# Kernel optimization log

Hardware: AMD Instinct MI355X
Metric: run time of the kernel (lower is better)

The kernel has to match this reference:

```python
import jax, jax.numpy as jnp
import numpy as np

EPS = 1e-07


def unfold(a, p):
    # torch F.unfold(a, p, padding=(p-1)//2, stride=1): [B,C,H,W] -> [B, C*p*p, H*W]
    B, C, H, W = a.shape
    pad = (p - 1) // 2
    ap = jnp.pad(a, ((0, 0), (0, 0), (pad, pad), (pad, pad)))
    # channel ordering is C-major then (kh, kw), matching torch unfold
    patches = jnp.stack([ap[:, :, i:i + H, j:j + W] for i in range(p) for j in range(p)], axis=2)
    return patches.reshape(B, C * p * p, H * W)


def linear_attn(q, k, x):
    # q:[B,h,l1,d1]  k:[B,h,l2,d1]  x:[B,h,l2,d2]
    l1, d1 = q.shape[-2:]
    l2, d2 = x.shape[-2:]
    kt = jnp.swapaxes(k, -2, -1)  # [B,h,d1,l2]
    if l1 * d1 * l2 + l1 * l2 * d2 <= d2 * l2 * d1 + d2 * d1 * l1:
        s = q @ kt                                        # [B,h,l1,l2]
        s = s / (s.sum(axis=-1, keepdims=True) + EPS)
        return s @ x
    else:
        out = q @ (kt @ x)                                # [B,h,l1,d2]
        denom = q @ kt.sum(axis=-1, keepdims=True) + EPS  # [B,h,l1,1]
        return out / denom


def setup_inputs() -> dict:
    key = jax.random.key(0)
    k1, k2, k3, k4, k5 = jax.random.split(key, 5)
    B, C, H, W = 4, 64, 128, 128
    x = jax.random.normal(k1, (B, C, H, W), dtype=jnp.float32)
    qkv_w = jax.random.normal(k2, (3 * C, C), dtype=jnp.float32) * 0.05
    qkv_b = jax.random.normal(k3, (3 * C,), dtype=jnp.float32) * 0.01
    proj_w = jax.random.normal(k4, (C, C, 3, 3), dtype=jnp.float32) * 0.05
    proj_b = jax.random.normal(k5, (C,), dtype=jnp.float32) * 0.01
    return {"x": x, "qkv_w": qkv_w, "qkv_b": qkv_b, "proj_w": proj_w, "proj_b": proj_b}


def reference(x, qkv_w, qkv_b, proj_w, proj_b):
    numHeads, patchSize = 8, 3
    B, C, H, W = x.shape
    L = H * W
    # 1x1 conv qkv
    qkv = jnp.einsum('bchw,oc->bohw', x, qkv_w) + qkv_b[None, :, None, None]
    q, k, v = qkv[:, :C], qkv[:, C:2 * C], qkv[:, 2 * C:]
    q = jax.nn.relu(q)
    k = jax.nn.relu(k)
    q = unfold(q, patchSize)  # [B, C*p*p, L]
    k = unfold(k, patchSize)
    v = v.reshape(B, C, L)
    d1 = C * patchSize * patchSize
    assert d1 % numHeads == 0  # chosen so replicate-pad branch is skipped
    q = jnp.swapaxes(q.reshape(B, numHeads, d1 // numHeads, L), -1, -2)   # [B,h,L,d1h]
    k = jnp.swapaxes(k.reshape(B, numHeads, d1 // numHeads, L), -1, -2)
    v = jnp.swapaxes(v.reshape(B, numHeads, C // numHeads, L), -1, -2)    # [B,h,L,d2h]
    out = linear_attn(q, k, v)                                            # [B,h,L,d2h]
    out = jnp.swapaxes(out, -1, -2).reshape(B, C, H, W)
    # 3x3 conv proj, padding 1
    out = jax.lax.conv_general_dilated(out, proj_w, window_strides=(1, 1), padding='SAME',
                                       dimension_numbers=('NCHW', 'OIHW', 'NCHW'))
    out = out + proj_b[None, :, None, None]
    return out
```

## Files before the change

### kernel.cpp

```cpp
#include <hip/hip_runtime.h>
#include <hip/hip_fp16.h>

#define LL 16384
#define HH 128
#define WW 128
#define CC 64
#define NH 8
#define EPSF 1e-7f
#define KVCHUNKS 32

typedef __attribute__((ext_vector_type(8))) _Float16 f16x8;
typedef __attribute__((ext_vector_type(4))) float f32x4;
typedef __attribute__((ext_vector_type(8))) unsigned short u16x8;

static __device__ __forceinline__ unsigned short f2h_bits(float v) {
    const _Float16 h = (_Float16)v;
    unsigned short b;
    __builtin_memcpy(&b, &h, 2);
    return b;
}
static __device__ __forceinline__ float h2f_u16(unsigned short s) {
    _Float16 h;
    __builtin_memcpy(&h, &s, 2);
    return (float)h;
}
static __device__ __forceinline__ float h2f_lo(unsigned int u) {
    return h2f_u16((unsigned short)(u & 0xffffu));
}
static __device__ __forceinline__ float h2f_hi(unsigned int u) {
    return h2f_u16((unsigned short)(u >> 16));
}

__global__ void qkv_kernel(const float* __restrict__ x, const float* __restrict__ w,
                           const float* __restrict__ bias,
                           unsigned short* __restrict__ q, unsigned short* __restrict__ k,
                           unsigned short* __restrict__ v) {
    const int pix0 = blockIdx.x * 128;
    const int b    = blockIdx.y;
    const int tid  = threadIdx.x;
    const int lane = tid & 63;
    const int wv   = tid >> 6;

    __shared__ _Float16 xh[128][72], xl[128][72];
    __shared__ unsigned short wspace[2 * 64 * 72];
    _Float16* whp = (_Float16*)wspace;
    _Float16* wlp = whp + 64 * 72;
    unsigned short* rep = wspace;

    {
        const float* xb = x + (size_t)b * CC * LL + pix0;
        for (int idx = tid; idx < 64 * 128; idx += 256) {
            const int ci = idx >> 7;
            const int px = idx & 127;
            const float vv = xb[(size_t)ci * LL + px];
            const _Float16 h = (_Float16)vv;
            xh[px][ci] = h;
            xl[px][ci] = (_Float16)(vv - (float)h);
        }
    }

    const int g8 = (lane >> 4) * 8;
    const int rl = lane & 15;

    for (int sec = 0; sec < 3; ++sec) {
        __syncthreads();
        {
            const float* wsec = w + (size_t)sec * 64 * 64;
            for (int idx = tid; idx < 64 * 64; idx += 256) {
                const int co = idx >> 6;
                const int ci = idx & 63;
                const float vv = wsec[co * 64 + ci];
                const _Float16 h = (_Float16)vv;
                whp[co * 72 + ci] = h;
                wlp[co * 72 + ci] = (_Float16)(vv - (float)h);
            }
        }
        __syncthreads();

        f32x4 acc[4][2];
#pragma unroll
        for (int ct = 0; ct < 4; ++ct)
#pragma unroll
            for (int pt = 0; pt < 2; ++pt) acc[ct][pt] = (f32x4)0.f;

#pragma unroll
        for (int ks = 0; ks < 2; ++ks) {
            const int kb = ks * 32 + g8;
            f16x8 ah[4], al[4], bh[2], bl[2];
#pragma unroll
            for (int ct = 0; ct < 4; ++ct) {
                ah[ct] = *(const f16x8*)&whp[(ct * 16 + rl) * 72 + kb];
                al[ct] = *(const f16x8*)&wlp[(ct * 16 + rl) * 72 + kb];
            }
#pragma unroll
            for (int pt = 0; pt < 2; ++pt) {
                bh[pt] = *(const f16x8*)&xh[wv * 32 + pt * 16 + rl][kb];
                bl[pt] = *(const f16x8*)&xl[wv * 32 + pt * 16 + rl][kb];
            }
#pragma unroll
            for (int ct = 0; ct < 4; ++ct)
#pragma unroll
                for (int pt = 0; pt < 2; ++pt) {
                    acc[ct][pt] = __builtin_amdgcn_mfma_f32_16x16x32_f16(ah[ct], bh[pt], acc[ct][pt], 0, 0, 0);
                    acc[ct][pt] = __builtin_amdgcn_mfma_f32_16x16x32_f16(ah[ct], bl[pt], acc[ct][pt], 0, 0, 0);
                    acc[ct][pt] = __builtin_amdgcn_mfma_f32_16x16x32_f16(al[ct], bh[pt], acc[ct][pt], 0, 0, 0);
                }
        }
        __syncthreads();

        const bool do_relu = (sec < 2);
#pragma unroll
        for (int ct = 0; ct < 4; ++ct) {
            const int co_b = ct * 16 + (lane >> 4) * 4;
#pragma unroll
            for (int pt = 0; pt < 2; ++pt) {
                const int pxl = wv * 32 + pt * 16 + rl;
#pragma unroll
                for (int j = 0; j < 4; ++j) {
                    const int co = co_b + j;
                    float val = acc[ct][pt][j] + bias[sec * 64 + co];
                    if (do_relu) val = fmaxf(val, 0.f);
                    rep[co * 128 + pxl] = f2h_bits(val);
                }
            }
        }
        __syncthreads();

        unsigned short* dst = ((sec == 0) ? q : (sec == 1) ? k : v) + (size_t)b * 64 * LL;
#pragma unroll
        for (int i = 0; i < 4; ++i) {
            const int slot = i * 256 + tid;
            const int co = slot >> 4;
            const int u4 = slot & 15;
            *(uint4*)(dst + (size_t)co * LL + pix0 + u4 * 8) = *(const uint4*)&rep[co * 128 + u4 * 8];
        }
    }
}

__global__ void kv_kernel(const unsigned short* __restrict__ k,
                          const unsigned short* __restrict__ v,
                          float* __restrict__ KVp) {
    const int chunk = blockIdx.x;
    const int h = blockIdx.y;
    const int b = blockIdx.z;
    const int tid = threadIdx.x;
    const int c  = tid >> 5;
    const int s  = tid & 31;
    const int half = s >> 4;
    const int sl   = s & 15;
    const int cpb  = half * 4;

    __shared__ float klds[8][6][130];

    {
        const unsigned short* kb = k + ((size_t)(b * 64) + 8 * h) * LL;
        for (int t = tid; t < 8 * 6 * 130; t += 256) {
            const int ch = t / 780;
            const int r1 = t - ch * 780;
            const int lr = r1 / 130;
            const int cx = r1 - lr * 130;
            const int gy = chunk * 4 + lr - 1;
            const int gx = cx - 1;
            const bool ok = (gy >= 0 && gy < HH && gx >= 0 && gx < WW);
            klds[ch][lr][cx] = ok ? h2f_u16(kb[(size_t)ch * LL + gy * WW + gx]) : 0.f;
        }
    }
    __syncthreads();

    const unsigned short* vbase = v + ((size_t)(b * 64) + 8 * h + cpb) * LL;

    float kv4[9][4] = {{0.f}};
    float ks[9] = {0.f};

    for (int r = 0; r < 4; ++r) {
        const int y = chunk * 4 + r;
        for (int g = 0; g < 4; ++g) {
            const int col0 = g * 32 + sl * 2;
            float va[4], vb2[4];
#pragma unroll
            for (int cp = 0; cp < 4; ++cp) {
                const unsigned int u = *(const unsigned int*)(vbase + (size_t)cp * LL + y * WW + col0);
                va[cp]  = h2f_lo(u);
                vb2[cp] = h2f_hi(u);
            }
            float kw[3][4];
#pragma unroll
            for (int dy = 0; dy < 3; ++dy)
#pragma unroll
                for (int dxx = 0; dxx < 4; ++dxx)
                    kw[dy][dxx] = klds[c][r + dy][col0 + dxx];
#pragma unroll
            for (int dy = 0; dy < 3; ++dy)
#pragma unroll
                for (int dx = 0; dx < 3; ++dx) {
                    const int p = dy * 3 + dx;
                    const float ka  = kw[dy][dx];
                    const float kb2 = kw[dy][dx + 1];
                    ks[p] += ka + kb2;
#pragma unroll
                    for (int cp = 0; cp < 4; ++cp)
                        kv4[p][cp] = fmaf(kb2, vb2[cp], fmaf(ka, va[cp], kv4[p][cp]));
                }
        }
    }

#pragma unroll
    for (int p = 0; p < 9; ++p) {
#pragma unroll
        for (int m = 8; m >= 1; m >>= 1) ks[p] += __shfl_xor(ks[p], m);
#pragma unroll
        for (int cp = 0; cp < 4; ++cp) {
#pragma unroll
            for (int m = 8; m >= 1; m >>= 1) kv4[p][cp] += __shfl_xor(kv4[p][cp], m);
        }
    }

    if (sl == 0) {
        float* dst = KVp + (((size_t)(b * NH + h) * KVCHUNKS) + chunk) * 648;
#pragma unroll
        for (int p = 0; p < 9; ++p) {
#pragma unroll
            for (int cp = 0; cp < 4; ++cp)
                dst[(c * 9 + p) * 8 + cpb + cp] = kv4[p][cp];
            if (half == 0) dst[576 + c * 9 + p] = ks[p];
        }
    }
}

__global__ void prep_kernel(const float* __restrict__ KVp,
                            float* __restrict__ KV, float* __restrict__ KS,
                            const float* __restrict__ w, unsigned short* __restrict__ wfrag) {
    if (blockIdx.x < 32) {
        const int bh = blockIdx.x;
        const float* src = KVp + (size_t)bh * KVCHUNKS * 648;
        for (int idx = threadIdx.x; idx < 648; idx += 256) {
            float s0 = 0.f, s1 = 0.f, s2 = 0.f, s3 = 0.f;
#pragma unroll
            for (int ch = 0; ch < KVCHUNKS; ch += 4) {
                s0 += src[(ch + 0) * 648 + idx];
                s1 += src[(ch + 1) * 648 + idx];
                s2 += src[(ch + 2) * 648 + idx];
                s3 += src[(ch + 3) * 648 + idx];
            }
            const float sum = (s0 + s1) + (s2 + s3);
            if (idx < 576) KV[(size_t)bh * 576 + idx] = sum;
            else           KS[(size_t)bh * 72 + (idx - 576)] = sum;
        }
    } else {
        const int idx = (blockIdx.x - 32) * 256 + threadIdx.x;
        const int kk = idx & 63;
        const int co = (idx >> 6) & 63;
        const int ks = idx >> 12;
        const int kg = ks * 64 + kk;
        const int ci = kg >> 4, tap = kg & 15;
        const float vv = (tap < 9) ? w[(co * 64 + ci) * 9 + tap] : 0.f;
        const int kx = (((kk >> 3) ^ (co & 7)) << 3) | (kk & 7);
        wfrag[((size_t)ks * 64 + co) * 64 + kx] = f2h_bits(vv);
    }
}

__global__ void attn_kernel(const unsigned short* __restrict__ q, const float* __restrict__ KV,
                            const float* __restrict__ KS, unsigned int* __restrict__ aofu) {
    const int y = blockIdx.x;
    const int h = blockIdx.y;
    const int b = blockIdx.z;
    const int t = threadIdx.x;

    float out0[8] = {0.f}, out1[8] = {0.f};
    float den0 = 0.f, den1 = 0.f;
    const int kvbase = (b * NH + h) * 8;
    const bool tlo = (t > 0), thi = (t < 63);

    for (int c = 0; c < 8; ++c) {
        const unsigned short* qc = q + ((size_t)(b * 64) + 8 * h + c) * LL;
        float qw[3][6];
#pragma unroll
        for (int dy = 0; dy < 3; ++dy) {
            const int yy = y + dy - 1;
            const bool yok = (yy >= 0 && yy < HH);
            const unsigned short* row = qc + yy * WW;
            const unsigned int u0 = (yok && tlo) ? *(const unsigned int*)(row + 2 * t - 2) : 0u;
            const unsigned int u1 = yok ? *(const unsigned int*)(row + 2 * t) : 0u;
            const unsigned int u2 = (yok && thi) ? *(const unsigned int*)(row + 2 * t + 2) : 0u;
            qw[dy][0] = h2f_lo(u0);  qw[dy][1] = h2f_hi(u0);
            qw[dy][2] = h2f_lo(u1);  qw[dy][3] = h2f_hi(u1);
            qw[dy][4] = h2f_lo(u2);  qw[dy][5] = h2f_hi(u2);
        }
        const float* kvr = KV + ((size_t)(kvbase + c) * 9) * 8;
        const float* ksr = KS + (size_t)(kvbase + c) * 9;
#pragma unroll
        for (int dy = 0; dy < 3; ++dy)
#pragma unroll
            for (int dx = 0; dx < 3; ++dx) {
                const int p = dy * 3 + dx;
                const float q0 = qw[dy][1 + dx];
                const float q1 = qw[dy][2 + dx];
                const float ksv = ksr[p];
                den0 = fmaf(q0, ksv, den0);
                den1 = fmaf(q1, ksv, den1);
#pragma unroll
                for (int cp = 0; cp < 8; ++cp) {
                    const float kvv = kvr[p * 8 + cp];
                    out0[cp] = fmaf(q0, kvv, out0[cp]);
                    out1[cp] = fmaf(q1, kvv, out1[cp]);
                }
            }
    }
    const float inv0 = 1.f / (den0 + EPSF);
    const float inv1 = 1.f / (den1 + EPSF);
    const int pixu = y * (WW / 2) + t;
#pragma unroll
    for (int cp = 0; cp < 8; ++cp) {
        const unsigned int lo = f2h_bits(out0[cp] * inv0);
        const unsigned int hi = f2h_bits(out1[cp] * inv1);
        aofu[((size_t)(b * 64) + h * 8 + cp) * (LL / 2) + pixu] = lo | (hi << 16);
    }
}

#define CONV_PREFETCH(KS)                                                        \
    do {                                                                         \
        if (tid < 128) {                                                         \
            const unsigned short* src_ = aofb + (size_t)((KS) * 4 + scis) * LL;  \
            pa0 = (oky0 && u0ok) ? *(const unsigned int*)(src_ + o_m - 2) : 0u;  \
            pa1 = oky0 ? *(const unsigned int*)(src_ + o_m) : 0u;                \
            pa2 = (oky0 && u2ok) ? *(const unsigned int*)(src_ + o_m + 2) : 0u;  \
            pb0 = u0ok ? *(const unsigned int*)(src_ + o_c - 2) : 0u;            \
            pb1 = *(const unsigned int*)(src_ + o_c);                            \
            pb2 = u2ok ? *(const unsigned int*)(src_ + o_c + 2) : 0u;            \
            pc0 = (oky2 && u0ok) ? *(const unsigned int*)(src_ + o_p - 2) : 0u;  \
            pc1 = oky2 ? *(const unsigned int*)(src_ + o_p) : 0u;                \
            pc2 = (oky2 && u2ok) ? *(const unsigned int*)(src_ + o_p + 2) : 0u;  \
        } else {                                                                 \
            const uint4* wsrc_ = (const uint4*)(wfrag + (size_t)(KS) * 4096);    \
            wf0 = wsrc_[wt];        wf1 = wsrc_[128 + wt];                       \
            wf2 = wsrc_[256 + wt];  wf3 = wsrc_[384 + wt];                       \
        }                                                                        \
    } while (0)

__global__ __launch_bounds__(256) void conv_kernel(const unsigned short* __restrict__ aof,
                                                   const unsigned short* __restrict__ wfrag,
                                                   const float* __restrict__ bias,
                                                   float* __restrict__ out) {
    const int bid = blockIdx.x;
    const int swz = (bid & 7) * 128 + (bid >> 3);
    const int b = swz >> 8;
    const int rem = swz & 255;
    const int y = rem >> 1;
    const int colbase = (rem & 1) * 64;
    const int tid = threadIdx.x;
    const int lane = tid & 63;
    const int wv = tid >> 6;
    const int rl = lane & 15;
    const int g  = lane >> 4;

    __shared__ unsigned short plds[2][64 * 64];
    __shared__ unsigned short wlds[2][64 * 64];

    f32x4 acc[4];
#pragma unroll
    for (int ct = 0; ct < 4; ++ct) acc[ct] = (f32x4)0.f;

    const int pair = tid & 31;
    const int scis = (tid >> 5) & 3;
    const int wt   = tid & 127;
    const int pxA  = pair * 2;
    const int pxB  = pxA + 1;

    const unsigned short* aofb = aof + (size_t)b * 64 * LL;
    const int xc0 = colbase + pxA;
    const int o_c = y * WW + xc0;
    const int o_m = o_c - WW;
    const int o_p = o_c + WW;
    const bool oky0 = (y > 0);
    const bool oky2 = (y < HH - 1);
    const bool u0ok = (xc0 >= 2);
    const bool u2ok = (xc0 + 3 < WW);
    const int xsA0 = (((2 * scis)     ^ (pxA & 7)) << 3);
    const int xsA1 = (((2 * scis + 1) ^ (pxA & 7)) << 3);
    const int xsB0 = (((2 * scis)     ^ (pxB & 7)) << 3);
    const int xsB1 = (((2 * scis + 1) ^ (pxB & 7)) << 3);

    unsigned int pa0, pa1, pa2, pb0, pb1, pb2, pc0, pc1, pc2;
    uint4 wf0, wf1, wf2, wf3;

    CONV_PREFETCH(0);

    for (int ks = 0; ks < 16; ++ks) {
        const int cur = ks & 1;
        if (tid < 128) {
            unsigned short ha[16], hb[16];
            ha[0] = (unsigned short)(pa0 >> 16);      ha[1] = (unsigned short)(pa1 & 0xffffu);  ha[2] = (unsigned short)(pa1 >> 16);
            ha[3] = (unsigned short)(pb0 >> 16);      ha[4] = (unsigned short)(pb1 & 0xffffu);  ha[5] = (unsigned short)(pb1 >> 16);
            ha[6] = (unsigned short)(pc0 >> 16);      ha[7] = (unsigned short)(pc1 & 0xffffu);  ha[8] = (unsigned short)(pc1 >> 16);
            hb[0] = (unsigned short)(pa1 & 0xffffu);  hb[1] = (unsigned short)(pa1 >> 16);      hb[2] = (unsigned short)(pa2 & 0xffffu);
            hb[3] = (unsigned short)(pb1 & 0xffffu);  hb[4] = (unsigned short)(pb1 >> 16);      hb[5] = (unsigned short)(pb2 & 0xffffu);
            hb[6] = (unsigned short)(pc1 & 0xffffu);  hb[7] = (unsigned short)(pc1 >> 16);      hb[8] = (unsigned short)(pc2 & 0xffffu);
#pragma unroll
            for (int j = 9; j < 16; ++j) { ha[j] = 0; hb[j] = 0; }
            *(u16x8*)&plds[cur][pxA * 64 + xsA0] = *(u16x8*)&ha[0];
            *(u16x8*)&plds[cur][pxA * 64 + xsA1] = *(u16x8*)&ha[8];
            *(u16x8*)&plds[cur][pxB * 64 + xsB0] = *(u16x8*)&hb[0];
            *(u16x8*)&plds[cur][pxB * 64 + xsB1] = *(u16x8*)&hb[8];
        } else {
            uint4* wdst = (uint4*)&wlds[cur][0];
            wdst[wt]        = wf0;
            wdst[128 + wt]  = wf1;
            wdst[256 + wt]  = wf2;
            wdst[384 + wt]  = wf3;
        }
        __syncthreads();
        if (ks < 15) CONV_PREFETCH(ks + 1);

#pragma unroll
        for (int ksub = 0; ksub < 2; ++ksub) {
            const int xs = (((ksub * 4 + g) ^ (rl & 7)) << 3);
            const int row = wv * 16 + rl;
            const f16x8 bh = *(const f16x8*)&plds[cur][row * 64 + xs];
#pragma unroll
            for (int ct = 0; ct < 4; ++ct) {
                const int rowa = ct * 16 + rl;
                const f16x8 ah = *(const f16x8*)&wlds[cur][rowa * 64 + xs];
                acc[ct] = __builtin_amdgcn_mfma_f32_16x16x32_f16(ah, bh, acc[ct], 0, 0, 0);
            }
        }
    }

#pragma unroll
    for (int ct = 0; ct < 4; ++ct) {
        const int co_b = ct * 16 + g * 4;
        const int px = colbase + wv * 16 + rl;
#pragma unroll
        for (int j = 0; j < 4; ++j) {
            const int co = co_b + j;
            out[((size_t)b * 64 + co) * LL + y * WW + px] = acc[ct][j] + bias[co];
        }
    }
}

extern "C" void kernel_launch(void* const* d_in, const int* in_sizes, int n_in,
                              void* d_out, int out_size, void* d_ws, size_t ws_size,
                              hipStream_t stream) {
    const float* x      = (const float*)d_in[0];
    const float* qkv_w  = (const float*)d_in[1];
    const float* qkv_b  = (const float*)d_in[2];
    const float* proj_w = (const float*)d_in[3];
    const float* proj_b = (const float*)d_in[4];
    float* out = (float*)d_out;
    float* ws  = (float*)d_ws;

    const size_t n1 = (size_t)4 * 64 * LL;
    unsigned short* qb  = (unsigned short*)ws;
    unsigned short* kb  = (unsigned short*)(ws + n1);
    unsigned short* vb  = (unsigned short*)(ws + 2 * n1);
    unsigned short* aof = (unsigned short*)(ws + 3 * n1);
    float* KV   = ws + 4 * n1;
    float* KS   = KV + 4 * 8 * 8 * 9 * 8;
    float* KVp  = KS + 4 * 8 * 8 * 9;
    unsigned short* wfrag = (unsigned short*)(KVp + (size_t)32 * KVCHUNKS * 648);

    qkv_kernel<<<dim3(128, 4), 256, 0, stream>>>(x, qkv_w, qkv_b, qb, kb, vb);
    kv_kernel<<<dim3(KVCHUNKS, NH, 4), 256, 0, stream>>>(kb, vb, KVp);
    prep_kernel<<<288, 256, 0, stream>>>(KVp, KV, KS, proj_w, wfrag);
    attn_kernel<<<dim3(128, NH, 4), 64, 0, stream>>>(qb, KV, KS, (unsigned int*)aof);
    conv_kernel<<<1024, 256, 0, stream>>>(aof, wfrag, proj_b, out);
}
```

Baseline: 96.96 us.

## Precompute split-fp16 QKV weights, vectorize x loads, reduce KV partials via atomics

```diff
diff --git a/kernel.cpp b/kernel.cpp
--- a/kernel.cpp
+++ b/kernel.cpp
@@ -31,7 +31,38 @@
     return h2f_u16((unsigned short)(u >> 16));
 }
 
-__global__ void qkv_kernel(const float* __restrict__ x, const float* __restrict__ w,
+__global__ void prep0_kernel(float* __restrict__ KVz,
+                             const float* __restrict__ pw, unsigned short* __restrict__ wfrag,
+                             const float* __restrict__ qw, unsigned short* __restrict__ wqkvf) {
+    const int bid = blockIdx.x;
+    if (bid < 81) {
+        KVz[bid * 256 + threadIdx.x] = 0.f;
+    } else if (bid < 337) {
+        const int idx = (bid - 81) * 256 + threadIdx.x;
+        const int kk = idx & 63;
+        const int co = (idx >> 6) & 63;
+        const int ks = idx >> 12;
+        const int kg = ks * 64 + kk;
+        const int ci = kg >> 4, tap = kg & 15;
+        const float vv = (tap < 9) ? pw[(co * 64 + ci) * 9 + tap] : 0.f;
+        const int kx = (((kk >> 3) ^ (co & 7)) << 3) | (kk & 7);
+        wfrag[((size_t)ks * 64 + co) * 64 + kx] = f2h_bits(vv);
+    } else {
+        const int idx = (bid - 337) * 256 + threadIdx.x;
+        const int hl = idx / 12288;
+        const int r  = idx - hl * 12288;
+        const int sec = r >> 12;
+        const int r2  = r & 4095;
+        const int co  = r2 >> 6;
+        const int ci  = r2 & 63;
+        const float vv = qw[(sec * 64 + co) * 64 + ci];
+        const _Float16 h = (_Float16)vv;
+        const float out = hl ? (vv - (float)h) : vv;
+        wqkvf[idx] = f2h_bits(out);
+    }
+}
+
+__global__ void qkv_kernel(const float* __restrict__ x, const unsigned short* __restrict__ wqkvf,
                            const float* __restrict__ bias,
                            unsigned short* __restrict__ q, unsigned short* __restrict__ k,
                            unsigned short* __restrict__ v) {
@@ -42,40 +73,36 @@
     const int wv   = tid >> 6;
 
     __shared__ _Float16 xh[128][72], xl[128][72];
-    __shared__ unsigned short wspace[2 * 64 * 72];
-    _Float16* whp = (_Float16*)wspace;
-    _Float16* wlp = whp + 64 * 72;
-    unsigned short* rep = wspace;
+    __shared__ unsigned short rep[64 * 128];
 
     {
         const float* xb = x + (size_t)b * CC * LL + pix0;
-        for (int idx = tid; idx < 64 * 128; idx += 256) {
-            const int ci = idx >> 7;
-            const int px = idx & 127;
-            const float vv = xb[(size_t)ci * LL + px];
-            const _Float16 h = (_Float16)vv;
-            xh[px][ci] = h;
-            xl[px][ci] = (_Float16)(vv - (float)h);
-        }
-    }
+        for (int i4 = tid; i4 < 2048; i4 += 256) {
+            const int ci = i4 >> 5;
+            const int px = (i4 & 31) * 4;
+            const float4 vv = *(const float4*)&xb[(size_t)ci * LL + px];
+            _Float16 h;
+            h = (_Float16)vv.x; xh[px + 0][ci] = h; xl[px + 0][ci] = (_Float16)(vv.x - (float)h);
+            h = (_Float16)vv.y; xh[px + 1][ci] = h; xl[px + 1][ci] = (_Float16)(vv.y - (float)h);
+            h = (_Float16)vv.z; xh[px + 2][ci] = h; xl[px + 2][ci] = (_Float16)(vv.z - (float)h);
+            h = (_Float16)vv.w; xh[px + 3][ci] = h; xl[px + 3][ci] = (_Float16)(vv.w - (float)h);
+        }
+    }
+    __syncthreads();
 
     const int g8 = (lane >> 4) * 8;
     const int rl = lane & 15;
 
     for (int sec = 0; sec < 3; ++sec) {
-        __syncthreads();
-        {
-            const float* wsec = w + (size_t)sec * 64 * 64;
-            for (int idx = tid; idx < 64 * 64; idx += 256) {
-                const int co = idx >> 6;
-                const int ci = idx & 63;
-                const float vv = wsec[co * 64 + ci];
-                const _Float16 h = (_Float16)vv;
-                whp[co * 72 + ci] = h;
-                wlp[co * 72 + ci] = (_Float16)(vv - (float)h);
-            }
-        }
-        __syncthreads();
+        f16x8 ah[4][2], al[4][2];
+#pragma unroll
+        for (int ct = 0; ct < 4; ++ct)
+#pragma unroll
+            for (int ks = 0; ks < 2; ++ks) {
+                const int off = sec * 4096 + (ct * 16 + rl) * 64 + ks * 32 + g8;
+                ah[ct][ks] = *(const f16x8*)&wqkvf[off];
+                al[ct][ks] = *(const f16x8*)&wqkvf[12288 + off];
+            }
 
         f32x4 acc[4][2];
 #pragma unroll
@@ -86,12 +113,7 @@
 #pragma unroll
         for (int ks = 0; ks < 2; ++ks) {
             const int kb = ks * 32 + g8;
-            f16x8 ah[4], al[4], bh[2], bl[2];
-#pragma unroll
-            for (int ct = 0; ct < 4; ++ct) {
-                ah[ct] = *(const f16x8*)&whp[(ct * 16 + rl) * 72 + kb];
-                al[ct] = *(const f16x8*)&wlp[(ct * 16 + rl) * 72 + kb];
-            }
+            f16x8 bh[2], bl[2];
 #pragma unroll
             for (int pt = 0; pt < 2; ++pt) {
                 bh[pt] = *(const f16x8*)&xh[wv * 32 + pt * 16 + rl][kb];
@@ -101,13 +123,13 @@
             for (int ct = 0; ct < 4; ++ct)
 #pragma unroll
                 for (int pt = 0; pt < 2; ++pt) {
-                    acc[ct][pt] = __builtin_amdgcn_mfma_f32_16x16x32_f16(ah[ct], bh[pt], acc[ct][pt], 0, 0, 0);
-                    acc[ct][pt] = __builtin_amdgcn_mfma_f32_16x16x32_f16(ah[ct], bl[pt], acc[ct][pt], 0, 0, 0);
-                    acc[ct][pt] = __builtin_amdgcn_mfma_f32_16x16x32_f16(al[ct], bh[pt], acc[ct][pt], 0, 0, 0);
+                    acc[ct][pt] = __builtin_amdgcn_mfma_f32_16x16x32_f16(ah[ct][ks], bh[pt], acc[ct][pt], 0, 0, 0);
+                    acc[ct][pt] = __builtin_amdgcn_mfma_f32_16x16x32_f16(ah[ct][ks], bl[pt], acc[ct][pt], 0, 0, 0);
+                    acc[ct][pt] = __builtin_amdgcn_mfma_f32_16x16x32_f16(al[ct][ks], bh[pt], acc[ct][pt], 0, 0, 0);
                 }
         }
+
         __syncthreads();
-
         const bool do_relu = (sec < 2);
 #pragma unroll
         for (int ct = 0; ct < 4; ++ct) {
@@ -139,7 +161,7 @@
 
 __global__ void kv_kernel(const unsigned short* __restrict__ k,
                           const unsigned short* __restrict__ v,
-                          float* __restrict__ KVp) {
+                          float* __restrict__ KV, float* __restrict__ KS) {
     const int chunk = blockIdx.x;
     const int h = blockIdx.y;
     const int b = blockIdx.z;
@@ -216,46 +238,15 @@
     }
 
     if (sl == 0) {
-        float* dst = KVp + (((size_t)(b * NH + h) * KVCHUNKS) + chunk) * 648;
+        const int bh = b * NH + h;
+        float* kvb = KV + (size_t)bh * 576;
 #pragma unroll
         for (int p = 0; p < 9; ++p) {
 #pragma unroll
             for (int cp = 0; cp < 4; ++cp)
-                dst[(c * 9 + p) * 8 + cpb + cp] = kv4[p][cp];
-            if (half == 0) dst[576 + c * 9 + p] = ks[p];
-        }
-    }
-}
-
-__global__ void prep_kernel(const float* __restrict__ KVp,
-                            float* __restrict__ KV, float* __restrict__ KS,
-                            const float* __restrict__ w, unsigned short* __restrict__ wfrag) {
-    if (blockIdx.x < 32) {
-        const int bh = blockIdx.x;
-        const float* src = KVp + (size_t)bh * KVCHUNKS * 648;
-        for (int idx = threadIdx.x; idx < 648; idx += 256) {
-            float s0 = 0.f, s1 = 0.f, s2 = 0.f, s3 = 0.f;
-#pragma unroll
-            for (int ch = 0; ch < KVCHUNKS; ch += 4) {
-                s0 += src[(ch + 0) * 648 + idx];
-                s1 += src[(ch + 1) * 648 + idx];
-                s2 += src[(ch + 2) * 648 + idx];
-                s3 += src[(ch + 3) * 648 + idx];
-            }
-            const float sum = (s0 + s1) + (s2 + s3);
-            if (idx < 576) KV[(size_t)bh * 576 + idx] = sum;
-            else           KS[(size_t)bh * 72 + (idx - 576)] = sum;
-        }
-    } else {
-        const int idx = (blockIdx.x - 32) * 256 + threadIdx.x;
-        const int kk = idx & 63;
-        const int co = (idx >> 6) & 63;
-        const int ks = idx >> 12;
-        const int kg = ks * 64 + kk;
-        const int ci = kg >> 4, tap = kg & 15;
-        const float vv = (tap < 9) ? w[(co * 64 + ci) * 9 + tap] : 0.f;
-        const int kx = (((kk >> 3) ^ (co & 7)) << 3) | (kk & 7);
-        wfrag[((size_t)ks * 64 + co) * 64 + kx] = f2h_bits(vv);
+                atomicAdd(&kvb[(c * 9 + p) * 8 + cpb + cp], kv4[p][cp]);
+            if (half == 0) atomicAdd(&KS[(size_t)bh * 72 + c * 9 + p], ks[p]);
+        }
     }
 }
 
@@ -454,13 +445,13 @@
     unsigned short* vb  = (unsigned short*)(ws + 2 * n1);
     unsigned short* aof = (unsigned short*)(ws + 3 * n1);
     float* KV   = ws + 4 * n1;
-    float* KS   = KV + 4 * 8 * 8 * 9 * 8;
-    float* KVp  = KS + 4 * 8 * 8 * 9;
-    unsigned short* wfrag = (unsigned short*)(KVp + (size_t)32 * KVCHUNKS * 648);
-
-    qkv_kernel<<<dim3(128, 4), 256, 0, stream>>>(x, qkv_w, qkv_b, qb, kb, vb);
-    kv_kernel<<<dim3(KVCHUNKS, NH, 4), 256, 0, stream>>>(kb, vb, KVp);
-    prep_kernel<<<288, 256, 0, stream>>>(KVp, KV, KS, proj_w, wfrag);
+    float* KS   = KV + 18432;
+    unsigned short* wfrag  = (unsigned short*)(KS + 2304);
+    unsigned short* wqkvf  = wfrag + 65536;
+
+    prep0_kernel<<<433, 256, 0, stream>>>(KV, proj_w, wfrag, qkv_w, wqkvf);
+    qkv_kernel<<<dim3(128, 4), 256, 0, stream>>>(x, wqkvf, qkv_b, qb, kb, vb);
+    kv_kernel<<<dim3(KVCHUNKS, NH, 4), 256, 0, stream>>>(kb, vb, KV, KS);
     attn_kernel<<<dim3(128, NH, 4), 64, 0, stream>>>(qb, KV, KS, (unsigned int*)aof);
     conv_kernel<<<1024, 256, 0, stream>>>(aof, wfrag, proj_b, out);
 }
```

After: 124.9 us. +28.8%, slower.
